# Kernel tuning notes

Hardware: AMD Instinct MI355X
Metric: run time of the kernel (lower is better)

The kernel has to match this reference:

```python
import jax, jax.numpy as jnp
import numpy as np


def setup_inputs() -> dict:
    key = jax.random.key(0)
    k1, k2 = jax.random.split(key)
    x = jax.random.normal(k1, (16, 2048, 256), dtype=jnp.float32)
    embed = jax.random.normal(k2, (1024, 256), dtype=jnp.float32)
    return {"x": x, "embed": embed}


def reference(x, embed):
    shape = x.shape
    xf = x.reshape(-1, shape[-1])  # (N, d)
    dist = -(jnp.sum(xf * xf, axis=1, keepdims=True)
             - 2.0 * (xf @ embed.T)
             + jnp.sum(embed * embed, axis=1)[None, :])  # (N, K)
    embed_ind = jnp.argmax(dist, axis=-1)  # (N,)
    embed_ind = embed_ind.reshape(shape[:-1])  # (B, T)
    quantize = embed[embed_ind]  # (B, T, d) gather
    return quantize, embed_ind
```

## Files before the change

### kernel.cpp

```cpp
#include <hip/hip_runtime.h>
#include <stdint.h>

#define NROWS 32768
#define DIMS  256
#define KCB   1024
#define BM 128
#define BN 128
#define GY (KCB/BN)
#define MARGIN 0.25f
#define CROWS 32

typedef _Float16 half8   __attribute__((ext_vector_type(8)));
typedef float    f32x4   __attribute__((ext_vector_type(4)));
typedef short    short4v __attribute__((ext_vector_type(4)));
typedef short    short8v __attribute__((ext_vector_type(8)));

__device__ __forceinline__ void gload_lds16(const void* g, void* l) {
    __builtin_amdgcn_global_load_lds(
        (const __attribute__((address_space(1))) uint32_t*)g,
        (__attribute__((address_space(3))) uint32_t*)l, 16, 0, 0);
}

__device__ __forceinline__ short f16h(float v) {
    _Float16 hh = (_Float16)v;
    return __builtin_bit_cast(short, hh);
}

__global__ __launch_bounds__(256) void xsplit(const float* __restrict__ x,
                                              short* __restrict__ Xh) {
    int T = blockIdx.x * 256 + threadIdx.x;
    int l = T & 63, c = (T >> 6) & 7, G = T >> 9;
    int row = G * 16 + (l & 15);
    int kb  = c * 32 + (l >> 4) * 8;
    const f32x4* src = (const f32x4*)(x + (size_t)row * DIMS + kb);
    f32x4 a = src[0], b = src[1];
    short8v h;
    #pragma unroll
    for (int e = 0; e < 4; ++e) { h[e] = f16h(a[e]); h[4 + e] = f16h(b[e]); }
    *(short8v*)(Xh + (size_t)G * 4096 + c * 512 + l * 8) = h;
}

__global__ __launch_bounds__(256) void esplit(const float* __restrict__ embed,
                                              short* __restrict__ Eh,
                                              float* __restrict__ he2) {
    int r = blockIdx.x * 4 + (threadIdx.x >> 6);
    int l = threadIdx.x & 63;
    f32x4 v = ((const f32x4*)(embed + (size_t)r * DIMS))[l];
    float s = v[0]*v[0] + v[1]*v[1] + v[2]*v[2] + v[3]*v[3];
    #pragma unroll
    for (int off = 32; off > 0; off >>= 1) s += __shfl_down(s, off, 64);
    if (l == 0) he2[r] = 0.5f * s;
    int G = r >> 4, cc = l >> 3;
    int fl = (r & 15) + 16 * ((l >> 1) & 3);
    size_t base = (size_t)G * 4096 + cc * 512 + fl * 8 + (l & 1) * 4;
    short4v h;
    #pragma unroll
    for (int e = 0; e < 4; ++e) h[e] = f16h(v[e]);
    *(short4v*)(Eh + base) = h;
}

__global__ __launch_bounds__(256, 4) void vq_mfma(
    const short* __restrict__ Xh, const short* __restrict__ Eh,
    const float* __restrict__ he2, float4* __restrict__ part)
{
    __shared__ char lds[32768];

    const int t = threadIdx.x, lane = t & 63, w = t >> 6;
    const int wm = w >> 1, wn = w & 1;
    const int lhi = lane >> 4, c15 = lane & 15;
    const int sid = blockIdx.x;
    const int xcd = sid & 7, j = sid >> 3;
    const int rb = xcd * 32 + (j >> 3), cb = j & 7;
    const int rowBase = rb * BM, colBase = cb * BN;

    const char* gA[4];
    const char* gB[4];
    #pragma unroll
    for (int m = 0; m < 4; ++m)
        gA[m] = (const char*)Xh + (size_t)(rb * 8 + wm * 4 + m) * 8192 + lane * 16;
    #pragma unroll
    for (int n = 0; n < 4; ++n)
        gB[n] = (const char*)Eh + (size_t)(cb * 8 + wn * 4 + n) * 8192 + lane * 16;
    char* lw = lds + w * 8192;

    f32x4 acc[4][4];
    #pragma unroll
    for (int m = 0; m < 4; ++m)
        #pragma unroll
        for (int n = 0; n < 4; ++n) acc[m][n] = (f32x4){0.f, 0.f, 0.f, 0.f};

    #pragma unroll
    for (int m = 0; m < 4; ++m) gload_lds16(gA[m], lw + m * 1024);
    #pragma unroll
    for (int n = 0; n < 4; ++n) gload_lds16(gB[n], lw + 4096 + n * 1024);

    #pragma unroll
    for (int c = 0; c < 8; ++c) {
        asm volatile("s_waitcnt vmcnt(0)" ::: "memory");
        __builtin_amdgcn_sched_barrier(0);

        half8 A[4], B[4];
        #pragma unroll
        for (int m = 0; m < 4; ++m)
            A[m] = *(const half8*)(lw + m * 1024 + lane * 16);
        #pragma unroll
        for (int n = 0; n < 4; ++n)
            B[n] = *(const half8*)(lw + 4096 + n * 1024 + lane * 16);
        asm volatile("s_waitcnt lgkmcnt(0)" ::: "memory");
        __builtin_amdgcn_sched_barrier(0);

        if (c < 7) {
            #pragma unroll
            for (int m = 0; m < 4; ++m)
                gload_lds16(gA[m] + (c + 1) * 1024, lw + m * 1024);
            #pragma unroll
            for (int n = 0; n < 4; ++n)
                gload_lds16(gB[n] + (c + 1) * 1024, lw + 4096 + n * 1024);
        }
        __builtin_amdgcn_sched_barrier(0);

        __builtin_amdgcn_s_setprio(1);
        #pragma unroll
        for (int m = 0; m < 4; ++m)
            #pragma unroll
            for (int n = 0; n < 4; ++n)
                acc[m][n] = __builtin_amdgcn_mfma_f32_16x16x32_f16(A[m], B[n], acc[m][n], 0, 0, 0);
        __builtin_amdgcn_s_setprio(0);
    }

    __syncthreads();
    float* S1 = (float*)lds;
    int*   I1 = (int*)(lds + 8704);
    float* S2 = (float*)(lds + 17408);

    float h2[4];
    #pragma unroll
    for (int n = 0; n < 4; ++n) h2[n] = he2[colBase + 64 * wn + 16 * n + c15];
    const int colg0 = colBase + 64 * wn + c15;

    #pragma unroll
    for (int m = 0; m < 4; ++m) {
        #pragma unroll
        for (int reg = 0; reg < 4; ++reg) {
            float b1 = acc[m][0][reg] - h2[0];
            int   i1 = colg0;
            float b2 = -3.4e38f;
            #pragma unroll
            for (int n = 1; n < 4; ++n) {
                float s = acc[m][n][reg] - h2[n];
                if (s > b1) { b2 = b1; b1 = s; i1 = colg0 + 16 * n; }
                else        { b2 = fmaxf(b2, s); }
            }
            {
                float ob1 = __shfl_xor(b1, 1, 64);
                int   oi1 = __shfl_xor(i1, 1, 64);
                float ob2 = __shfl_xor(b2, 1, 64);
                if (ob1 > b1 || (ob1 == b1 && oi1 < i1)) {
                    b2 = fmaxf(b1, ob2); b1 = ob1; i1 = oi1;
                } else {
                    b2 = fmaxf(b2, ob1);
                }
            }
            if ((c15 & 1) == 0) {
                int row  = 64 * wm + 16 * m + 4 * lhi + reg;
                int slot = wn * 8 + (c15 >> 1);
                S1[row * 17 + slot] = b1;
                I1[row * 17 + slot] = i1;
                S2[row * 17 + slot] = b2;
            }
        }
    }
    __syncthreads();

    if (t < BM) {
        float b1 = S1[t * 17]; int i1 = I1[t * 17]; float b2 = S2[t * 17];
        #pragma unroll
        for (int s = 1; s < 16; ++s) {
            float c1 = S1[t * 17 + s]; int j1 = I1[t * 17 + s];
            float c2 = S2[t * 17 + s];
            if (c1 > b1 || (c1 == b1 && j1 < i1)) { b2 = fmaxf(b1, c2); b1 = c1; i1 = j1; }
            else                                  { b2 = fmaxf(b2, c1); }
        }
        part[(size_t)(rowBase + t) * GY + cb] =
            make_float4(b1, __int_as_float(i1), b2, 0.f);
    }
}

__device__ __forceinline__ float dot16(f32x4 xa, f32x4 xb, f32x4 xc, f32x4 xd,
                                       const float* __restrict__ erow, int q) {
    const f32x4* er = (const f32x4*)(erow + q * 16);
    f32x4 ea = er[0], eb = er[1], ec = er[2], ed = er[3];
    float s = xa[0] * ea[0];
    s = fmaf(xa[1], ea[1], s); s = fmaf(xa[2], ea[2], s); s = fmaf(xa[3], ea[3], s);
    s = fmaf(xb[0], eb[0], s); s = fmaf(xb[1], eb[1], s);
    s = fmaf(xb[2], eb[2], s); s = fmaf(xb[3], eb[3], s);
    s = fmaf(xc[0], ec[0], s); s = fmaf(xc[1], ec[1], s);
    s = fmaf(xc[2], ec[2], s); s = fmaf(xc[3], ec[3], s);
    s = fmaf(xd[0], ed[0], s); s = fmaf(xd[1], ed[1], s);
    s = fmaf(xd[2], ed[2], s); s = fmaf(xd[3], ed[3], s);
    s += __shfl_xor(s, 1, 64);
    s += __shfl_xor(s, 2, 64);
    s += __shfl_xor(s, 4, 64);
    s += __shfl_xor(s, 8, 64);
    return s;
}

__global__ __launch_bounds__(256) void vq_combine(
    const float4* __restrict__ part, const float* __restrict__ embed,
    const float* __restrict__ x, const float* __restrict__ he2,
    float* __restrict__ outq, float* __restrict__ outi)
{
    __shared__ int idxS[CROWS];
    __shared__ int flagL[CROWS];
    __shared__ int flagN;
    const int t = threadIdx.x, l = t & 63, w = t >> 6;
    const int rowBase = blockIdx.x * CROWS;

    if (t == 0) flagN = 0;
    __syncthreads();

    if (t < CROWS) {
        const int row = rowBase + t;
        float4 p = part[(size_t)row * GY];
        float b1 = p.x; int i1 = __float_as_int(p.y); float b2 = p.z;
        #pragma unroll
        for (int g = 1; g < GY; ++g) {
            float4 q = part[(size_t)row * GY + g];
            float c1 = q.x; int j1 = __float_as_int(q.y); float c2 = q.z;
            if (c1 > b1 || (c1 == b1 && j1 < i1)) { b2 = fmaxf(b1, c2); b1 = c1; i1 = j1; }
            else                                  { b2 = fmaxf(b2, c1); }
        }
        idxS[t] = i1;
        outi[row] = (float)i1;
        if (b1 - b2 < MARGIN) {
            int s = atomicAdd(&flagN, 1);
            flagL[s] = t;
        }
    }
    __syncthreads();

    #pragma unroll
    for (int qq = 0; qq < (CROWS * 64) / 256; ++qq) {
        int f = t + 256 * qq;
        int r = f >> 6, c4 = f & 63;
        int e = idxS[r];
        f32x4 v = *(const f32x4*)(embed + (size_t)e * DIMS + c4 * 4);
        *(f32x4*)(outq + (size_t)(rowBase + r) * DIMS + c4 * 4) = v;
    }
    __syncthreads();

    const int nf = flagN;
    const int q = l & 15, pgrp = l >> 4;
    for (int it = w; it < nf; it += 4) {
        int rrow = rowBase + flagL[it];
        const f32x4* xr = (const f32x4*)(x + (size_t)rrow * DIMS + q * 16);
        f32x4 xa = xr[0], xb = xr[1], xc = xr[2], xd = xr[3];

        float4 pc[GY];
        #pragma unroll
        for (int g = 0; g < GY; ++g) pc[g] = part[(size_t)rrow * GY + g];
        float B1 = pc[0].x;
        #pragma unroll
        for (int g = 1; g < GY; ++g) B1 = fmaxf(B1, pc[g].x);
        const float T = B1 - MARGIN;

        float wb = -3.4e38f; int wi = 0x7fffffff;
        #pragma unroll
        for (int g = 0; g < GY; ++g) {
            if (pc[g].z >= T) {
                #pragma unroll 2
                for (int i = 0; i < BN / 4; ++i) {
                    int code = g * BN + i * 4 + pgrp;
                    float s = dot16(xa, xb, xc, xd,
                                    embed + (size_t)code * DIMS, q) - he2[code];
                    if (s > wb || (s == wb && code < wi)) { wb = s; wi = code; }
                }
            } else if (pc[g].x >= T) {
                int code = __float_as_int(pc[g].y);
                float s = dot16(xa, xb, xc, xd,
                                embed + (size_t)code * DIMS, q) - he2[code];
                if (s > wb || (s == wb && code < wi)) { wb = s; wi = code; }
            }
        }
        #pragma unroll
        for (int msk = 16; msk <= 32; msk <<= 1) {
            float ob = __shfl_xor(wb, msk, 64);
            int   oi = __shfl_xor(wi, msk, 64);
            if (ob > wb || (ob == wb && oi < wi)) { wb = ob; wi = oi; }
        }
        f32x4 v = ((const f32x4*)(embed + (size_t)wi * DIMS))[l];
        ((f32x4*)(outq + (size_t)rrow * DIMS))[l] = v;
        if (l == 0) outi[rrow] = (float)wi;
    }
}

extern "C" void kernel_launch(void* const* d_in, const int* in_sizes, int n_in,
                              void* d_out, int out_size, void* d_ws, size_t ws_size,
                              hipStream_t stream) {
    const float* x     = (const float*)d_in[0];
    const float* embed = (const float*)d_in[1];
    char* ws = (char*)d_ws;
    float*  he2  = (float*)ws;
    float4* part = (float4*)(ws + 8192);
    short*  Xh   = (short*)(ws + 8192 + 4194304);
    short*  Eh   = (short*)(ws + 8192 + 4194304 + 16777216);
    float*  out  = (float*)d_out;
    float*  outi = out + (size_t)NROWS * DIMS;

    xsplit<<<4096, 256, 0, stream>>>(x, Xh);
    esplit<<<KCB / 4, 256, 0, stream>>>(embed, Eh, he2);
    vq_mfma<<<(NROWS / BM) * GY, 256, 0, stream>>>(Xh, Eh, he2, part);
    vq_combine<<<NROWS / CROWS, 256, 0, stream>>>(part, embed, x, he2, out, outi);
}
```

Baseline: 73.87 us.

## Double-buffer LDS in VQ MFMA loop, merge split kernels, shrink combine rows

Result: slower. 79.95 us (+8.2%).

```diff
diff --git a/kernel.cpp b/kernel.cpp
--- a/kernel.cpp
+++ b/kernel.cpp
@@ -8,7 +8,7 @@
 #define BN 128
 #define GY (KCB/BN)
 #define MARGIN 0.25f
-#define CROWS 32
+#define CROWS 16
 
 typedef _Float16 half8   __attribute__((ext_vector_type(8)));
 typedef float    f32x4   __attribute__((ext_vector_type(4)));
@@ -26,44 +26,45 @@
     return __builtin_bit_cast(short, hh);
 }
 
-__global__ __launch_bounds__(256) void xsplit(const float* __restrict__ x,
-                                              short* __restrict__ Xh) {
-    int T = blockIdx.x * 256 + threadIdx.x;
-    int l = T & 63, c = (T >> 6) & 7, G = T >> 9;
-    int row = G * 16 + (l & 15);
-    int kb  = c * 32 + (l >> 4) * 8;
-    const f32x4* src = (const f32x4*)(x + (size_t)row * DIMS + kb);
-    f32x4 a = src[0], b = src[1];
-    short8v h;
-    #pragma unroll
-    for (int e = 0; e < 4; ++e) { h[e] = f16h(a[e]); h[4 + e] = f16h(b[e]); }
-    *(short8v*)(Xh + (size_t)G * 4096 + c * 512 + l * 8) = h;
-}
-
-__global__ __launch_bounds__(256) void esplit(const float* __restrict__ embed,
-                                              short* __restrict__ Eh,
-                                              float* __restrict__ he2) {
-    int r = blockIdx.x * 4 + (threadIdx.x >> 6);
-    int l = threadIdx.x & 63;
-    f32x4 v = ((const f32x4*)(embed + (size_t)r * DIMS))[l];
-    float s = v[0]*v[0] + v[1]*v[1] + v[2]*v[2] + v[3]*v[3];
-    #pragma unroll
-    for (int off = 32; off > 0; off >>= 1) s += __shfl_down(s, off, 64);
-    if (l == 0) he2[r] = 0.5f * s;
-    int G = r >> 4, cc = l >> 3;
-    int fl = (r & 15) + 16 * ((l >> 1) & 3);
-    size_t base = (size_t)G * 4096 + cc * 512 + fl * 8 + (l & 1) * 4;
-    short4v h;
-    #pragma unroll
-    for (int e = 0; e < 4; ++e) h[e] = f16h(v[e]);
-    *(short4v*)(Eh + base) = h;
-}
-
-__global__ __launch_bounds__(256, 4) void vq_mfma(
+__global__ __launch_bounds__(256) void split_all(
+    const float* __restrict__ x, short* __restrict__ Xh,
+    const float* __restrict__ embed, short* __restrict__ Eh,
+    float* __restrict__ he2)
+{
+    if (blockIdx.x < 4096) {
+        int T = blockIdx.x * 256 + threadIdx.x;
+        int l = T & 63, c = (T >> 6) & 7, G = T >> 9;
+        int row = G * 16 + (l & 15);
+        int kb  = c * 32 + (l >> 4) * 8;
+        const f32x4* src = (const f32x4*)(x + (size_t)row * DIMS + kb);
+        f32x4 a = src[0], b = src[1];
+        short8v h;
+        #pragma unroll
+        for (int e = 0; e < 4; ++e) { h[e] = f16h(a[e]); h[4 + e] = f16h(b[e]); }
+        *(short8v*)(Xh + (size_t)G * 4096 + c * 512 + l * 8) = h;
+    } else {
+        int r = (blockIdx.x - 4096) * 4 + (threadIdx.x >> 6);
+        int l = threadIdx.x & 63;
+        f32x4 v = ((const f32x4*)(embed + (size_t)r * DIMS))[l];
+        float s = v[0]*v[0] + v[1]*v[1] + v[2]*v[2] + v[3]*v[3];
+        #pragma unroll
+        for (int off = 32; off > 0; off >>= 1) s += __shfl_down(s, off, 64);
+        if (l == 0) he2[r] = 0.5f * s;
+        int G = r >> 4, cc = l >> 3;
+        int fl = (r & 15) + 16 * ((l >> 1) & 3);
+        size_t base = (size_t)G * 4096 + cc * 512 + fl * 8 + (l & 1) * 4;
+        short4v h;
+        #pragma unroll
+        for (int e = 0; e < 4; ++e) h[e] = f16h(v[e]);
+        *(short4v*)(Eh + base) = h;
+    }
+}
+
+__global__ __launch_bounds__(256, 2) void vq_mfma(
     const short* __restrict__ Xh, const short* __restrict__ Eh,
     const float* __restrict__ he2, float4* __restrict__ part)
 {
-    __shared__ char lds[32768];
+    __shared__ char lds[65536];
 
     const int t = threadIdx.x, lane = t & 63, w = t >> 6;
     const int wm = w >> 1, wn = w & 1;
@@ -81,7 +82,7 @@
     #pragma unroll
     for (int n = 0; n < 4; ++n)
         gB[n] = (const char*)Eh + (size_t)(cb * 8 + wn * 4 + n) * 8192 + lane * 16;
-    char* lw = lds + w * 8192;
+    char* lw = lds + w * 16384;
 
     f32x4 acc[4][4];
     #pragma unroll
@@ -93,29 +94,35 @@
     for (int m = 0; m < 4; ++m) gload_lds16(gA[m], lw + m * 1024);
     #pragma unroll
     for (int n = 0; n < 4; ++n) gload_lds16(gB[n], lw + 4096 + n * 1024);
+    #pragma unroll
+    for (int m = 0; m < 4; ++m) gload_lds16(gA[m] + 1024, lw + 8192 + m * 1024);
+    #pragma unroll
+    for (int n = 0; n < 4; ++n) gload_lds16(gB[n] + 1024, lw + 8192 + 4096 + n * 1024);
 
     #pragma unroll
     for (int c = 0; c < 8; ++c) {
-        asm volatile("s_waitcnt vmcnt(0)" ::: "memory");
+        if (c < 7) asm volatile("s_waitcnt vmcnt(8)" ::: "memory");
+        else       asm volatile("s_waitcnt vmcnt(0)" ::: "memory");
         __builtin_amdgcn_sched_barrier(0);
 
+        const char* buf = lw + (c & 1) * 8192;
         half8 A[4], B[4];
         #pragma unroll
         for (int m = 0; m < 4; ++m)
-            A[m] = *(const half8*)(lw + m * 1024 + lane * 16);
+            A[m] = *(const half8*)(buf + m * 1024 + lane * 16);
         #pragma unroll
         for (int n = 0; n < 4; ++n)
-            B[n] = *(const half8*)(lw + 4096 + n * 1024 + lane * 16);
+            B[n] = *(const half8*)(buf + 4096 + n * 1024 + lane * 16);
         asm volatile("s_waitcnt lgkmcnt(0)" ::: "memory");
         __builtin_amdgcn_sched_barrier(0);
 
-        if (c < 7) {
+        if (c < 6) {
             #pragma unroll
             for (int m = 0; m < 4; ++m)
-                gload_lds16(gA[m] + (c + 1) * 1024, lw + m * 1024);
+                gload_lds16(gA[m] + (c + 2) * 1024, lw + (c & 1) * 8192 + m * 1024);
             #pragma unroll
             for (int n = 0; n < 4; ++n)
-                gload_lds16(gB[n] + (c + 1) * 1024, lw + 4096 + n * 1024);
+                gload_lds16(gB[n] + (c + 2) * 1024, lw + (c & 1) * 8192 + 4096 + n * 1024);
         }
         __builtin_amdgcn_sched_barrier(0);
 
@@ -307,8 +314,7 @@
     float*  out  = (float*)d_out;
     float*  outi = out + (size_t)NROWS * DIMS;
 
-    xsplit<<<4096, 256, 0, stream>>>(x, Xh);
-    esplit<<<KCB / 4, 256, 0, stream>>>(embed, Eh, he2);
+    split_all<<<4352, 256, 0, stream>>>(x, Xh, embed, Eh, he2);
     vq_mfma<<<(NROWS / BM) * GY, 256, 0, stream>>>(Xh, Eh, he2, part);
     vq_combine<<<NROWS / CROWS, 256, 0, stream>>>(part, embed, x, he2, out, outi);
 }
```
